# Kernel optimization log

Measured on AMD Instinct MI355X. Metric: run time of the kernel, lower is better.

Reference implementation:

```python
import jax, jax.numpy as jnp
import numpy as np

B, S, E = 2, 4096, 1024
QD, VD = 64, 64
WIN, DIL = 5, 2


def setup_inputs() -> dict:
    key = jax.random.key(0)
    ks = jax.random.split(key, 7)
    sc = E ** -0.5  # linear-layer init scale
    return {
        "x": jax.random.normal(ks[0], (B, S, E), jnp.float32),
        "Wq": jax.random.normal(ks[1], (E, QD), jnp.float32) * sc,
        "bq": jnp.zeros((QD,), jnp.float32),
        "Wk": jax.random.normal(ks[2], (E, QD), jnp.float32) * sc,
        "bk": jnp.zeros((QD,), jnp.float32),
        "Wv": jax.random.normal(ks[3], (E, VD), jnp.float32) * sc,
        "bv": jnp.zeros((VD,), jnp.float32),
    }


def reference(x, Wq, bq, Wk, bk, Wv, bv):
    b, s, _ = x.shape
    Q = x @ Wq + bq  # (b, s, QD)
    K = x @ Wk + bk  # (b, s, QD)
    V = x @ Wv + bv  # (b, s, VD)

    half = WIN // 2
    offsets = DIL * (jnp.arange(WIN) - half)
    i = jnp.arange(s)                                  # (s,)
    j = i[None, :] + offsets[:, None]
    valid = (j >= 0) & (j < s)                         # in-range band entries
    jc = jnp.clip(j, 0, s - 1)

    Kg = K[:, jc, :]
    # per-offset diagonal dot products Q_i . K_{i+d}
    c = jnp.einsum('bsd,bwsd->bws', Q, Kg) * valid

    ib = jnp.broadcast_to(i[None, :], (WIN, s))
    # Banded score matrix, zeros off-band (as in the original: torch.zeros scatter).
    # Masked (invalid) entries add 0, so clipped index collisions are harmless.
    scores = jnp.zeros((b, s, s), x.dtype).at[:, ib, jc].add(c)

    attn = jax.nn.softmax(scores, axis=2)              # softmax over full row incl. zeros
    return attn @ V                                    # (b, s, VD)
```

## Files before the change

### kernel.cpp

```cpp
#include <hip/hip_runtime.h>
#include <hip/hip_bf16.h>

typedef __hip_bfloat16 bf16;
typedef short bf16x8 __attribute__((ext_vector_type(8)));
typedef float f32x4 __attribute__((ext_vector_type(4)));

#define S_LEN 4096
#define NBATCH 2
#define EDIM 1024
#define DDIM 64
#define MROWS (NBATCH * S_LEN)
#define KPHASE 512

union frag_u { bf16x8 v; bf16 e[8]; };

__device__ inline void cvt_split(const float4& a, const float4& b,
                                 bf16x8& hi, bf16x8& lo) {
  float v[8] = {a.x, a.y, a.z, a.w, b.x, b.y, b.z, b.w};
  frag_u h, l;
#pragma unroll
  for (int e = 0; e < 8; e++) {
    bf16 hh = __float2bfloat16(v[e]);
    h.e[e] = hh;
    l.e[e] = __float2bfloat16(v[e] - __bfloat162float(hh));
  }
  hi = h.v;
  lo = l.v;
}

__global__ __launch_bounds__(256) void pack_w_kernel(
    const float* __restrict__ Wq, const float* __restrict__ Wk,
    const float* __restrict__ Wv, bf16* __restrict__ Wt_hi,
    bf16* __restrict__ Wt_lo, float* __restrict__ Vsum) {
  int idx = blockIdx.x * 256 + threadIdx.x;
  if (blockIdx.x == 0 && threadIdx.x < NBATCH * DDIM) Vsum[threadIdx.x] = 0.f;
  int mat = idx >> 16;
  int rem = idx & 65535;
  int n = rem >> 10;
  int k = rem & 1023;
  const float* W = (mat == 0) ? Wq : ((mat == 1) ? Wk : Wv);
  float v = W[k * DDIM + n];
  bf16 h = __float2bfloat16(v);
  Wt_hi[idx] = h;
  Wt_lo[idx] = __float2bfloat16(v - __bfloat162float(h));
}

__global__ __launch_bounds__(512, 2) void qkv_gemm_kernel(
    const float* __restrict__ x, const bf16* __restrict__ Wt_hi,
    const bf16* __restrict__ Wt_lo, const float* __restrict__ bq,
    const float* __restrict__ bk, const float* __restrict__ bv,
    float* __restrict__ qkv) {
  __shared__ float lds_red[32 * 192];
  const int tid = threadIdx.x;
  const int lane = tid & 63;
  const int wave = tid >> 6;
  const int quad = lane >> 4;
  const int l16 = lane & 15;
  const int kphase = wave >> 2;
  const int nw = wave & 3;
  const int rowBase = blockIdx.x * 32;
  const int kbase = kphase * KPHASE;

  const float* xa0 = x + (size_t)(rowBase + l16) * EDIM + quad * 8 + kbase;
  const float* xa1 = xa0 + (size_t)16 * EDIM;
  size_t boff[3];
#pragma unroll
  for (int t = 0; t < 3; t++)
    boff[t] = (size_t)((nw * 3 + t) * 16 + l16) * EDIM + quad * 8 + kbase;

  f32x4 acc[2][3];
#pragma unroll
  for (int mt = 0; mt < 2; mt++)
#pragma unroll
    for (int t = 0; t < 3; t++) acc[mt][t] = (f32x4){0.f, 0.f, 0.f, 0.f};

  float4 cx[4];
  bf16x8 cbh[3], cbl[3];
  cx[0] = *(const float4*)(const void*)(xa0);
  cx[1] = *(const float4*)(const void*)(xa0 + 4);
  cx[2] = *(const float4*)(const void*)(xa1);
  cx[3] = *(const float4*)(const void*)(xa1 + 4);
#pragma unroll
  for (int t = 0; t < 3; t++) {
    cbh[t] = *(const bf16x8*)(const void*)(Wt_hi + boff[t]);
    cbl[t] = *(const bf16x8*)(const void*)(Wt_lo + boff[t]);
  }

  for (int k0 = 0; k0 < KPHASE; k0 += 32) {
    const bool more = (k0 + 32) < KPHASE;
    float4 nx[4];
    bf16x8 nbh[3], nbl[3];
    if (more) {
      int k1 = k0 + 32;
      nx[0] = *(const float4*)(const void*)(xa0 + k1);
      nx[1] = *(const float4*)(const void*)(xa0 + k1 + 4);
      nx[2] = *(const float4*)(const void*)(xa1 + k1);
      nx[3] = *(const float4*)(const void*)(xa1 + k1 + 4);
#pragma unroll
      for (int t = 0; t < 3; t++) {
        nbh[t] = *(const bf16x8*)(const void*)(Wt_hi + boff[t] + k1);
        nbl[t] = *(const bf16x8*)(const void*)(Wt_lo + boff[t] + k1);
      }
    }

    bf16x8 ah0, al0, ah1, al1;
    cvt_split(cx[0], cx[1], ah0, al0);
    cvt_split(cx[2], cx[3], ah1, al1);
#pragma unroll
    for (int t = 0; t < 3; t++) {
      acc[0][t] = __builtin_amdgcn_mfma_f32_16x16x32_bf16(ah0, cbh[t], acc[0][t], 0, 0, 0);
      acc[1][t] = __builtin_amdgcn_mfma_f32_16x16x32_bf16(ah1, cbh[t], acc[1][t], 0, 0, 0);
      acc[0][t] = __builtin_amdgcn_mfma_f32_16x16x32_bf16(ah0, cbl[t], acc[0][t], 0, 0, 0);
      acc[1][t] = __builtin_amdgcn_mfma_f32_16x16x32_bf16(ah1, cbl[t], acc[1][t], 0, 0, 0);
      acc[0][t] = __builtin_amdgcn_mfma_f32_16x16x32_bf16(al0, cbh[t], acc[0][t], 0, 0, 0);
      acc[1][t] = __builtin_amdgcn_mfma_f32_16x16x32_bf16(al1, cbh[t], acc[1][t], 0, 0, 0);
    }

    if (more) {
#pragma unroll
      for (int j = 0; j < 4; j++) cx[j] = nx[j];
#pragma unroll
      for (int t = 0; t < 3; t++) {
        cbh[t] = nbh[t];
        cbl[t] = nbl[t];
      }
    }
  }

  if (kphase == 1) {
#pragma unroll
    for (int mt = 0; mt < 2; mt++)
#pragma unroll
      for (int t = 0; t < 3; t++) {
        int n = (nw * 3 + t) * 16 + l16;
#pragma unroll
        for (int r = 0; r < 4; r++) {
          int row = mt * 16 + quad * 4 + r;
          lds_red[row * 192 + n] = acc[mt][t][r];
        }
      }
  }
  __syncthreads();
  if (kphase == 0) {
#pragma unroll
    for (int mt = 0; mt < 2; mt++)
#pragma unroll
      for (int t = 0; t < 3; t++) {
        int n = (nw * 3 + t) * 16 + l16;
        int mat = n >> 6;
        int col = n & 63;
        float bias = (mat == 0) ? bq[col] : ((mat == 1) ? bk[col] : bv[col]);
        float* dst = qkv + (size_t)mat * MROWS * DDIM +
                     (size_t)(rowBase + mt * 16 + quad * 4) * DDIM + col;
#pragma unroll
        for (int r = 0; r < 4; r++) {
          int row = mt * 16 + quad * 4 + r;
          dst[r * DDIM] = acc[mt][t][r] + lds_red[row * 192 + n] + bias;
        }
      }
  }
}

__global__ __launch_bounds__(256) void vsum_kernel(const float* __restrict__ Vf,
                                                   float* __restrict__ Vsum) {
  int b = blockIdx.x >> 5;
  int chunk = blockIdx.x & 31;
  int col = threadIdx.x & 63;
  int rg = threadIdx.x >> 6;
  const float* base =
      Vf + ((size_t)b * S_LEN + chunk * 128 + rg * 32) * DDIM + col;
  float s = 0.f;
#pragma unroll
  for (int r = 0; r < 32; r++) s += base[r * DDIM];
  __shared__ float red[256];
  red[threadIdx.x] = s;
  __syncthreads();
  if (threadIdx.x < 64)
    atomicAdd(&Vsum[b * DDIM + col],
              red[col] + red[col + 64] + red[col + 128] + red[col + 192]);
}

__global__ __launch_bounds__(256) void attn_kernel(
    const float* __restrict__ Qf, const float* __restrict__ Kf,
    const float* __restrict__ Vf, const float* __restrict__ Vsum,
    float* __restrict__ out) {
  int l = threadIdx.x & 31;
  int qidx = blockIdx.x * 8 + (threadIdx.x >> 5);
  int b = qidx >> 12;
  int i = qidx & 4095;

  float2 q = *(const float2*)(const void*)(Qf + (size_t)qidx * DDIM + 2 * l);
  float sc[5];
  float2 vv[5];
  bool val[5];
#pragma unroll
  for (int w = 0; w < 5; w++) {
    int j = i + 2 * w - 4;
    val[w] = (j >= 0) && (j < S_LEN);
    int jj = val[w] ? j : i;
    size_t off = (size_t)(b * S_LEN + jj) * DDIM + 2 * l;
    float2 kk = *(const float2*)(const void*)(Kf + off);
    vv[w] = *(const float2*)(const void*)(Vf + off);
    float p = q.x * kk.x + q.y * kk.y;
#pragma unroll
    for (int d = 1; d < 32; d <<= 1) p += __shfl_xor(p, d, 64);
    sc[w] = p;
  }

  float mx = 0.f;
#pragma unroll
  for (int w = 0; w < 5; w++)
    if (val[w]) mx = fmaxf(mx, sc[w]);

  float denom = 0.f;
  float2 accv = {0.f, 0.f}, vsel = {0.f, 0.f};
  int nval = 0;
#pragma unroll
  for (int w = 0; w < 5; w++)
    if (val[w]) {
      float p = __expf(sc[w] - mx);
      denom += p;
      accv.x += p * vv[w].x;
      accv.y += p * vv[w].y;
      vsel.x += vv[w].x;
      vsel.y += vv[w].y;
      nval++;
    }
  float p0 = __expf(-mx);
  denom += p0 * (float)(S_LEN - nval);
  float2 vs = *(const float2*)(const void*)(Vsum + b * DDIM + 2 * l);
  accv.x += p0 * (vs.x - vsel.x);
  accv.y += p0 * (vs.y - vsel.y);

  float2 o = {accv.x / denom, accv.y / denom};
  *(float2*)(void*)(out + (size_t)qidx * DDIM + 2 * l) = o;
}

extern "C" void kernel_launch(void* const* d_in, const int* in_sizes, int n_in,
                              void* d_out, int out_size, void* d_ws,
                              size_t ws_size, hipStream_t stream) {
  const float* x = (const float*)d_in[0];
  const float* Wq = (const float*)d_in[1];
  const float* bq = (const float*)d_in[2];
  const float* Wk = (const float*)d_in[3];
  const float* bk = (const float*)d_in[4];
  const float* Wv = (const float*)d_in[5];
  const float* bv = (const float*)d_in[6];
  float* out = (float*)d_out;

  char* ws = (char*)d_ws;
  bf16* Wt_hi = (bf16*)ws;
  bf16* Wt_lo = (bf16*)(ws + 393216);
  float* qkv = (float*)(ws + 786432);
  float* Qf = qkv;
  float* Kf = qkv + (size_t)MROWS * DDIM;
  float* Vf = Kf + (size_t)MROWS * DDIM;
  float* Vsum = (float*)(ws + 786432 + 6291456);

  hipLaunchKernelGGL(pack_w_kernel, dim3(768), dim3(256), 0, stream, Wq, Wk, Wv,
                     Wt_hi, Wt_lo, Vsum);
  hipLaunchKernelGGL(qkv_gemm_kernel, dim3(256), dim3(512), 0, stream, x, Wt_hi,
                     Wt_lo, bq, bk, bv, qkv);
  hipLaunchKernelGGL(vsum_kernel, dim3(64), dim3(256), 0, stream, Vf, Vsum);
  hipLaunchKernelGGL(attn_kernel, dim3(1024), dim3(256), 0, stream, Qf, Kf, Vf,
                     Vsum, out);
}
```

Before: 125.0 us.

## Stage x tiles in LDS via async global_load_lds and transpose W through LDS

The QKV GEMM now loads x into an XOR-swizzled LDS buffer using async global-to-LDS loads, 64 columns per k-step in each of two K halves. Each wave now owns a 16-row by 96-column tile, and the W fragments are read straight from global memory without register double-buffering. The weight pack kernel now transposes through a padded LDS tile so that reads and bf16x8 writes are both coalesced, using 48 blocks instead of 768. The aim is to replace uncoalesced strided access with wide coalesced access. The cost is two barriers per k-step and no prefetch of B, which can expose load latency.

```diff
diff --git a/kernel.cpp b/kernel.cpp
--- a/kernel.cpp
+++ b/kernel.cpp
@@ -10,12 +10,19 @@
 #define EDIM 1024
 #define DDIM 64
 #define MROWS (NBATCH * S_LEN)
-#define KPHASE 512
+
+#define GLOBAL_AS __attribute__((address_space(1)))
+#define LDS_AS __attribute__((address_space(3)))
 
 union frag_u { bf16x8 v; bf16 e[8]; };
 
-__device__ inline void cvt_split(const float4& a, const float4& b,
-                                 bf16x8& hi, bf16x8& lo) {
+__device__ __forceinline__ void async_ld16(const float* gp, float* lp) {
+  __builtin_amdgcn_global_load_lds((const GLOBAL_AS void*)gp,
+                                   (LDS_AS void*)lp, 16, 0, 0);
+}
+
+__device__ __forceinline__ void cvt_split(const float4& a, const float4& b,
+                                          bf16x8& hi, bf16x8& lo) {
   float v[8] = {a.x, a.y, a.z, a.w, b.x, b.y, b.z, b.w};
   frag_u h, l;
 #pragma unroll
@@ -32,17 +39,45 @@
     const float* __restrict__ Wq, const float* __restrict__ Wk,
     const float* __restrict__ Wv, bf16* __restrict__ Wt_hi,
     bf16* __restrict__ Wt_lo, float* __restrict__ Vsum) {
-  int idx = blockIdx.x * 256 + threadIdx.x;
-  if (blockIdx.x == 0 && threadIdx.x < NBATCH * DDIM) Vsum[threadIdx.x] = 0.f;
-  int mat = idx >> 16;
-  int rem = idx & 65535;
-  int n = rem >> 10;
-  int k = rem & 1023;
+  __shared__ float tile[64 * 65];
+  const int mat = blockIdx.x >> 4;
+  const int kb = (blockIdx.x & 15) * 64;
+  const int t = threadIdx.x;
+  if (blockIdx.x == 0 && t < NBATCH * DDIM) Vsum[t] = 0.f;
   const float* W = (mat == 0) ? Wq : ((mat == 1) ? Wk : Wv);
-  float v = W[k * DDIM + n];
-  bf16 h = __float2bfloat16(v);
-  Wt_hi[idx] = h;
-  Wt_lo[idx] = __float2bfloat16(v - __bfloat162float(h));
+
+#pragma unroll
+  for (int i = 0; i < 4; i++) {
+    int F = (i * 256 + t) * 4;
+    int k = F >> 6;
+    int n4 = F & 63;
+    float4 v = *(const float4*)(const void*)(W + (size_t)(kb + k) * 64 + n4);
+    tile[(n4 + 0) * 65 + k] = v.x;
+    tile[(n4 + 1) * 65 + k] = v.y;
+    tile[(n4 + 2) * 65 + k] = v.z;
+    tile[(n4 + 3) * 65 + k] = v.w;
+  }
+  __syncthreads();
+
+  const int n = t >> 2;
+  const int kc = (t & 3) * 16;
+  frag_u h0, h1, l0, l1;
+#pragma unroll
+  for (int e = 0; e < 8; e++) {
+    float v0 = tile[n * 65 + kc + e];
+    float v1 = tile[n * 65 + kc + 8 + e];
+    bf16 a = __float2bfloat16(v0);
+    bf16 b = __float2bfloat16(v1);
+    h0.e[e] = a;
+    h1.e[e] = b;
+    l0.e[e] = __float2bfloat16(v0 - __bfloat162float(a));
+    l1.e[e] = __float2bfloat16(v1 - __bfloat162float(b));
+  }
+  size_t obase = (size_t)(mat * 64 + n) * EDIM + kb + kc;
+  *(bf16x8*)(void*)(Wt_hi + obase) = h0.v;
+  *(bf16x8*)(void*)(Wt_hi + obase + 8) = h1.v;
+  *(bf16x8*)(void*)(Wt_lo + obase) = l0.v;
+  *(bf16x8*)(void*)(Wt_lo + obase + 8) = l1.v;
 }
 
 __global__ __launch_bounds__(512, 2) void qkv_gemm_kernel(
@@ -50,114 +85,93 @@
     const bf16* __restrict__ Wt_lo, const float* __restrict__ bq,
     const float* __restrict__ bk, const float* __restrict__ bv,
     float* __restrict__ qkv) {
-  __shared__ float lds_red[32 * 192];
+  __shared__ float lds[6144];
   const int tid = threadIdx.x;
   const int lane = tid & 63;
   const int wave = tid >> 6;
   const int quad = lane >> 4;
   const int l16 = lane & 15;
-  const int kphase = wave >> 2;
-  const int nw = wave & 3;
+  const int p = wave >> 2;
+  const int mh = (wave >> 1) & 1;
+  const int nw = wave & 1;
   const int rowBase = blockIdx.x * 32;
-  const int kbase = kphase * KPHASE;
-
-  const float* xa0 = x + (size_t)(rowBase + l16) * EDIM + quad * 8 + kbase;
-  const float* xa1 = xa0 + (size_t)16 * EDIM;
-  size_t boff[3];
-#pragma unroll
-  for (int t = 0; t < 3; t++)
-    boff[t] = (size_t)((nw * 3 + t) * 16 + l16) * EDIM + quad * 8 + kbase;
-
-  f32x4 acc[2][3];
-#pragma unroll
-  for (int mt = 0; mt < 2; mt++)
-#pragma unroll
-    for (int t = 0; t < 3; t++) acc[mt][t] = (f32x4){0.f, 0.f, 0.f, 0.f};
-
-  float4 cx[4];
-  bf16x8 cbh[3], cbl[3];
-  cx[0] = *(const float4*)(const void*)(xa0);
-  cx[1] = *(const float4*)(const void*)(xa0 + 4);
-  cx[2] = *(const float4*)(const void*)(xa1);
-  cx[3] = *(const float4*)(const void*)(xa1 + 4);
-#pragma unroll
-  for (int t = 0; t < 3; t++) {
-    cbh[t] = *(const bf16x8*)(const void*)(Wt_hi + boff[t]);
-    cbl[t] = *(const bf16x8*)(const void*)(Wt_lo + boff[t]);
-  }
-
-  for (int k0 = 0; k0 < KPHASE; k0 += 32) {
-    const bool more = (k0 + 32) < KPHASE;
-    float4 nx[4];
-    bf16x8 nbh[3], nbl[3];
-    if (more) {
-      int k1 = k0 + 32;
-      nx[0] = *(const float4*)(const void*)(xa0 + k1);
-      nx[1] = *(const float4*)(const void*)(xa0 + k1 + 4);
-      nx[2] = *(const float4*)(const void*)(xa1 + k1);
-      nx[3] = *(const float4*)(const void*)(xa1 + k1 + 4);
-#pragma unroll
-      for (int t = 0; t < 3; t++) {
-        nbh[t] = *(const bf16x8*)(const void*)(Wt_hi + boff[t] + k1);
-        nbl[t] = *(const bf16x8*)(const void*)(Wt_lo + boff[t] + k1);
+  const int rA = mh * 16 + l16;
+
+  int s0 = wave * 256 + lane * 4;
+  int s1 = 2048 + wave * 256 + lane * 4;
+  int r0 = s0 >> 7, pc0 = s0 & 127;
+  int r1 = s1 >> 7, pc1 = s1 & 127;
+  int c0 = ((((pc0 >> 3) ^ (r0 & 7)) << 3) | (pc0 & 7));
+  int c1 = ((((pc1 >> 3) ^ (r1 & 7)) << 3) | (pc1 & 7));
+  const float* gsrc0 = x + (size_t)(rowBase + r0) * EDIM + (c0 >> 6) * 512 + (c0 & 63);
+  const float* gsrc1 = x + (size_t)(rowBase + r1) * EDIM + (c1 >> 6) * 512 + (c1 & 63);
+  float* ldst0 = &lds[wave * 256];
+  float* ldst1 = &lds[2048 + wave * 256];
+
+  int bidx[6];
+#pragma unroll
+  for (int t = 0; t < 6; t++)
+    bidx[t] = ((nw * 6 + t) * 16 + l16) * EDIM + quad * 8 + p * 512;
+
+  f32x4 acc[6];
+#pragma unroll
+  for (int t = 0; t < 6; t++) acc[t] = (f32x4){0.f, 0.f, 0.f, 0.f};
+
+  for (int j = 0; j < 8; j++) {
+    if (j) __syncthreads();
+    async_ld16(gsrc0 + j * 64, ldst0);
+    async_ld16(gsrc1 + j * 64, ldst1);
+    __syncthreads();
+
+#pragma unroll
+    for (int u = 0; u < 2; u++) {
+      int cc = p * 64 + u * 32 + quad * 8;
+      int gsw = ((cc >> 3) ^ (rA & 7));
+      const float* aptr = &lds[rA * 128 + gsw * 8];
+      float4 a0 = *(const float4*)(const void*)aptr;
+      float4 a1 = *(const float4*)(const void*)(aptr + 4);
+      bf16x8 ah, al;
+      cvt_split(a0, a1, ah, al);
+      int koff = j * 64 + u * 32;
+#pragma unroll
+      for (int t = 0; t < 6; t++) {
+        bf16x8 bh = *(const bf16x8*)(const void*)(Wt_hi + bidx[t] + koff);
+        bf16x8 bl = *(const bf16x8*)(const void*)(Wt_lo + bidx[t] + koff);
+        acc[t] = __builtin_amdgcn_mfma_f32_16x16x32_bf16(ah, bh, acc[t], 0, 0, 0);
+        acc[t] = __builtin_amdgcn_mfma_f32_16x16x32_bf16(ah, bl, acc[t], 0, 0, 0);
+        acc[t] = __builtin_amdgcn_mfma_f32_16x16x32_bf16(al, bh, acc[t], 0, 0, 0);
       }
     }
-
-    bf16x8 ah0, al0, ah1, al1;
-    cvt_split(cx[0], cx[1], ah0, al0);
-    cvt_split(cx[2], cx[3], ah1, al1);
-#pragma unroll
-    for (int t = 0; t < 3; t++) {
-      acc[0][t] = __builtin_amdgcn_mfma_f32_16x16x32_bf16(ah0, cbh[t], acc[0][t], 0, 0, 0);
-      acc[1][t] = __builtin_amdgcn_mfma_f32_16x16x32_bf16(ah1, cbh[t], acc[1][t], 0, 0, 0);
-      acc[0][t] = __builtin_amdgcn_mfma_f32_16x16x32_bf16(ah0, cbl[t], acc[0][t], 0, 0, 0);
-      acc[1][t] = __builtin_amdgcn_mfma_f32_16x16x32_bf16(ah1, cbl[t], acc[1][t], 0, 0, 0);
-      acc[0][t] = __builtin_amdgcn_mfma_f32_16x16x32_bf16(al0, cbh[t], acc[0][t], 0, 0, 0);
-      acc[1][t] = __builtin_amdgcn_mfma_f32_16x16x32_bf16(al1, cbh[t], acc[1][t], 0, 0, 0);
-    }
-
-    if (more) {
-#pragma unroll
-      for (int j = 0; j < 4; j++) cx[j] = nx[j];
-#pragma unroll
-      for (int t = 0; t < 3; t++) {
-        cbh[t] = nbh[t];
-        cbl[t] = nbl[t];
+  }
+
+  __syncthreads();
+  if (p == 1) {
+#pragma unroll
+    for (int t = 0; t < 6; t++) {
+      int n = (nw * 6 + t) * 16 + l16;
+#pragma unroll
+      for (int r = 0; r < 4; r++) {
+        int row = mh * 16 + quad * 4 + r;
+        lds[row * 192 + n] = acc[t][r];
       }
     }
   }
-
-  if (kphase == 1) {
-#pragma unroll
-    for (int mt = 0; mt < 2; mt++)
-#pragma unroll
-      for (int t = 0; t < 3; t++) {
-        int n = (nw * 3 + t) * 16 + l16;
-#pragma unroll
-        for (int r = 0; r < 4; r++) {
-          int row = mt * 16 + quad * 4 + r;
-          lds_red[row * 192 + n] = acc[mt][t][r];
-        }
+  __syncthreads();
+  if (p == 0) {
+#pragma unroll
+    for (int t = 0; t < 6; t++) {
+      int n = (nw * 6 + t) * 16 + l16;
+      int mat = n >> 6;
+      int col = n & 63;
+      float bias = (mat == 0) ? bq[col] : ((mat == 1) ? bk[col] : bv[col]);
+      float* dst = qkv + (size_t)mat * MROWS * DDIM +
+                   (size_t)(rowBase + mh * 16 + quad * 4) * DDIM + col;
+#pragma unroll
+      for (int r = 0; r < 4; r++) {
+        int row = mh * 16 + quad * 4 + r;
+        dst[r * DDIM] = acc[t][r] + lds[row * 192 + n] + bias;
       }
-  }
-  __syncthreads();
-  if (kphase == 0) {
-#pragma unroll
-    for (int mt = 0; mt < 2; mt++)
-#pragma unroll
-      for (int t = 0; t < 3; t++) {
-        int n = (nw * 3 + t) * 16 + l16;
-        int mat = n >> 6;
-        int col = n & 63;
-        float bias = (mat == 0) ? bq[col] : ((mat == 1) ? bk[col] : bv[col]);
-        float* dst = qkv + (size_t)mat * MROWS * DDIM +
-                     (size_t)(rowBase + mt * 16 + quad * 4) * DDIM + col;
-#pragma unroll
-        for (int r = 0; r < 4; r++) {
-          int row = mt * 16 + quad * 4 + r;
-          dst[r * DDIM] = acc[mt][t][r] + lds_red[row * 192 + n] + bias;
-        }
-      }
+    }
   }
 }
 
@@ -218,10 +232,10 @@
 #pragma unroll
   for (int w = 0; w < 5; w++)
     if (val[w]) {
-      float p = __expf(sc[w] - mx);
-      denom += p;
-      accv.x += p * vv[w].x;
-      accv.y += p * vv[w].y;
+      float pexp = __expf(sc[w] - mx);
+      denom += pexp;
+      accv.x += pexp * vv[w].x;
+      accv.y += pexp * vv[w].y;
       vsel.x += vv[w].x;
       vsel.y += vv[w].y;
       nval++;
@@ -257,7 +271,7 @@
   float* Vf = Kf + (size_t)MROWS * DDIM;
   float* Vsum = (float*)(ws + 786432 + 6291456);
 
-  hipLaunchKernelGGL(pack_w_kernel, dim3(768), dim3(256), 0, stream, Wq, Wk, Wv,
+  hipLaunchKernelGGL(pack_w_kernel, dim3(48), dim3(256), 0, stream, Wq, Wk, Wv,
                      Wt_hi, Wt_lo, Vsum);
   hipLaunchKernelGGL(qkv_gemm_kernel, dim3(256), dim3(512), 0, stream, x, Wt_hi,
                      Wt_lo, bq, bk, bv, qkv);
```

New measurement: 139.5 us. +11.6%, slower.
